# Kernel tuning notes

Measured on AMD Instinct MI355X. Metric: run time of the kernel, lower is better.

Reference implementation:

```python
import jax, jax.numpy as jnp
import numpy as np

P, M, N, H, B, E, K = 50, 512, 1024, 256, 8, 400, 5
ALPHA_MAX, TAU_MAX, RHO_MAX, ETA_MAX = 0.01, 1.0, 1.0, 1.0
LEAK = 0.01  # F.leaky_relu default slope


def _lrelu(x):
    return jnp.where(x >= 0, x, LEAK * x)


def _layernorm(x, g, b, eps=1e-5):
    mu = jnp.mean(x, axis=-1, keepdims=True)
    var = jnp.mean((x - mu) ** 2, axis=-1, keepdims=True)
    return (x - mu) * jax.lax.rsqrt(var + eps) * g + b


def setup_inputs() -> dict:
    ks = iter(jax.random.split(jax.random.key(0), 16))

    def w(fin, fout):
        return jax.random.normal(next(ks), (fin, fout), jnp.float32) * np.float32(np.sqrt(2.0 / (fin + fout)))

    H4 = 4 * H
    inp = {
        'A': jax.random.normal(next(ks), (1, P, M, N), jnp.float32) * 0.05,
        'b': jax.random.normal(next(ks), (B, P, M, 1), jnp.float32),
        'W1': w(2 * N, H), 'b1': jnp.zeros(H), 'bn1_s': jnp.ones(H), 'bn1_t': jnp.zeros(H),
        'W2': w(H, 2 * H), 'b2': jnp.zeros(2 * H), 'bn2_s': jnp.ones(2 * H), 'bn2_t': jnp.zeros(2 * H),
        'W3': w(2 * H, H4), 'b3': jnp.zeros(H4), 'bn3_s': jnp.ones(H4), 'bn3_t': jnp.zeros(H4),
        'W4': w(H4, H4), 'b4': jnp.zeros(H4), 'bn4_s': jnp.ones(H4), 'bn4_t': jnp.zeros(H4),
        'W5': w(H4, H4), 'b5': jnp.zeros(H4), 'bn5_s': jnp.ones(H4), 'bn5_t': jnp.zeros(H4),
        'ln_g': jnp.ones(H4), 'ln_b': jnp.zeros(H4),
        'Wd1': w(P * H4, H4), 'bd1': jnp.zeros(H4), 'lnd1_g': jnp.ones(H4), 'lnd1_b': jnp.zeros(H4),
        'Wd2': w(H4, 2 * H), 'bd2': jnp.zeros(2 * H), 'lnd2_g': jnp.ones(2 * H), 'lnd2_b': jnp.zeros(2 * H),
        'Wd3': w(2 * H, H), 'bd3': jnp.zeros(H), 'lnd3_g': jnp.ones(H), 'lnd3_b': jnp.zeros(H),
        'Wfc': w(H, 4) * 0.1, 'bfc': jnp.zeros(4),
        'edge_index': jax.random.randint(next(ks), (2, E), 0, P),
    }
    return inp


def reference(A, b, W1, b1, bn1_s, bn1_t, W2, b2, bn2_s, bn2_t, W3, b3, bn3_s, bn3_t,
              W4, b4, bn4_s, bn4_t, W5, b5, bn5_s, bn5_t, ln_g, ln_b,
              Wd1, bd1, lnd1_g, lnd1_b, Wd2, bd2, lnd2_g, lnd2_b, Wd3, bd3, lnd3_g, lnd3_b,
              Wfc, bfc, edge_index):
    A0 = A[0]                                             # [P,M,N]
    AtA = jnp.einsum('pmi,pmj->pij', A0, A0)              # [P,N,N]  (compute_Atx(A))
    Atb = jnp.einsum('pmn,bpm->bpn', A0, b[..., 0])[..., None]  # [B,P,N,1]

    src, dst = edge_index[0], edge_index[1]
    ones_e = jnp.ones((E,), A.dtype)
    # sum_neighbors: out-degree of each node p, shape broadcastable to [B,P,1,1]
    sum_nb = jax.ops.segment_sum(ones_e, src, num_segments=P)[None, :, None, None]

    # GCNConv normalization with self loops: norm_ij = deg_i^-1/2 * deg_j^-1/2
    sl = jnp.arange(P)
    src_a = jnp.concatenate([src, sl])
    dst_a = jnp.concatenate([dst, sl])
    deg = jax.ops.segment_sum(jnp.ones((E + P,), A.dtype), dst_a, num_segments=P)
    dinv = jax.lax.rsqrt(deg)
    coef = (dinv[src_a] * dinv[dst_a])[:, None]           # [E+P,1]

    convs = [(W1, b1, bn1_s, bn1_t), (W2, b2, bn2_s, bn2_t), (W3, b3, bn3_s, bn3_t),
             (W4, b4, bn4_s, bn4_t), (W5, b5, bn5_s, bn5_t)]

    def gconv(x, W, bias):                                # x: [P,Cin]
        xw = x @ W
        return jax.ops.segment_sum(xw[src_a] * coef, dst_a, num_segments=P) + bias

    def encode_one(feat):                                 # feat: [P,2N]
        x = feat
        for (W, bias, s, t) in convs:
            # leaky_relu -> BatchNorm1d (eval: affine scale/shift) -> dropout (eval: id)
            x = _lrelu(gconv(x, W, bias)) * s + t
        return _layernorm(x, ln_g, ln_b).reshape(-1)      # [P*4H]

    enc = jax.vmap(encode_one)

    y = jnp.zeros((B, P, N, 1), A.dtype)
    U = jnp.zeros_like(y)
    delta = jnp.zeros_like(y)
    Ys = []
    for k in range(K):
        AtAy = jnp.einsum('pij,bpj->bpi', AtA, y[..., 0])[..., None]  # [B,P,N,1]
        feat = jnp.concatenate([AtAy, Atb], axis=2)[..., 0]           # [B,P,2N]
        code = enc(feat)                                              # [B,P*4H]
        h = _lrelu(_layernorm(code @ Wd1 + bd1, lnd1_g, lnd1_b))
        h = _lrelu(_layernorm(h @ Wd2 + bd2, lnd2_g, lnd2_b))
        h = _lrelu(_layernorm(h @ Wd3 + bd3, lnd3_g, lnd3_b))
        hyp = jnp.clip(jax.nn.sigmoid(h @ Wfc + bfc), 1e-4, 0.99).reshape(B, 4, 1, 1, 1)
        alpha = hyp[:, 0] * ALPHA_MAX
        tau = hyp[:, 1] * TAU_MAX
        rho = hyp[:, 2] * RHO_MAX
        eta = hyp[:, 3] * ETA_MAX
        g = AtAy - Atb + jnp.sign(y) * tau + U * sum_nb + delta * rho
        mg = max(30.0, 100.0 - k)
        g = jnp.clip(g, -mg, mg)
        mv = max(10.0, 200.0 - k * 3)
        y = jnp.clip(y - alpha * g, -mv, mv)
        # compute_delta: for each directed edge (s,d): delta[s]+= (y_s-y_d); delta[d]-= (y_s-y_d)
        diff = y[:, src] - y[:, dst]                                  # [B,E,N,1]
        delta = jnp.zeros_like(y).at[:, src].add(diff).at[:, dst].add(-diff)
        U = jnp.clip(U + delta * eta, -mv, mv)
        Ys.append(y)
    return jnp.stack(Ys)                                              # [K,B,P,N,1]
```

## Files before the change

### kernel.cpp

```cpp
#include <hip/hip_runtime.h>

#define PP 50
#define MM 512
#define NN 1024

constexpr size_t F_ATB   = 0;
constexpr size_t F_ATAY  = F_ATB   + 409600;
constexpr size_t F_Y     = F_ATAY  + 409600;
constexpr size_t F_U     = F_Y     + 409600;
constexpr size_t F_DELTA = F_U     + 409600;
constexpr size_t F_BT    = F_DELTA + 409600;
constexpr size_t F_AYT   = F_BT    + 204800;
constexpr size_t F_ZA    = F_AYT   + 204800;
constexpr size_t F_ZB    = F_ZA    + 458752;
constexpr size_t F_X0    = F_ZB    + 458752;
constexpr size_t F_X1    = F_X0    + 409600;
constexpr size_t F_CODET = F_X1    + 409600;
constexpr size_t F_PART  = F_CODET + 409600;
constexpr size_t F_DPART2= F_PART  + 3670016;
constexpr size_t F_H1    = F_DPART2+ 32768;
constexpr size_t F_H2    = F_H1    + 8192;
constexpr size_t F_H3    = F_H2    + 4096;
constexpr size_t F_HYP   = F_H3    + 2048;
constexpr size_t F_GCCO  = F_HYP   + 64;
constexpr size_t F_SUMNB = F_GCCO  + 512;
constexpr size_t F_W1B   = F_SUMNB + 64;
constexpr size_t F_END   = F_W1B   + 102400;

__device__ __forceinline__ float lrelu(float v) { return v >= 0.f ? v : 0.01f * v; }

__device__ __forceinline__ void bred2(float& s1, float& s2, float* sm) {
  #pragma unroll
  for (int off = 32; off > 0; off >>= 1) {
    s1 += __shfl_down(s1, off);
    s2 += __shfl_down(s2, off);
  }
  int w = threadIdx.x >> 6, l = threadIdx.x & 63;
  if (l == 0) { sm[w] = s1; sm[4 + w] = s2; }
  __syncthreads();
  s1 = sm[0] + sm[1] + sm[2] + sm[3];
  s2 = sm[4] + sm[5] + sm[6] + sm[7];
}

__global__ __launch_bounds__(512) void ksetup(const int* __restrict__ ei, float* sumnb,
                                              float* gccoef, int* gcoff, int* gcsrc,
                                              int* nbroff, int* nbridx) {
  __shared__ int cin[PP];
  __shared__ int cou[PP];
  __shared__ float sdinv[PP];
  __shared__ int goff[PP + 1], noff[PP + 1];
  int t = threadIdx.x;
  const int* src = ei;
  const int* dst = ei + 400;
  if (t < PP) { cin[t] = 0; cou[t] = 0; }
  __syncthreads();
  if (t < 400) {
    atomicAdd(&cou[src[t]], 1);
    atomicAdd(&cin[dst[t]], 1);
  }
  __syncthreads();
  if (t < PP) {
    sdinv[t] = rsqrtf((float)(cin[t] + 1));
    sumnb[t] = (float)cou[t];
  }
  __syncthreads();
  if (t == 0) {
    goff[0] = 0; noff[0] = 0;
    for (int p = 0; p < PP; ++p) {
      goff[p + 1] = goff[p] + cin[p] + 1;
      noff[p + 1] = noff[p] + cin[p] + cou[p];
    }
  }
  __syncthreads();
  if (t <= PP) { gcoff[t] = goff[t]; nbroff[t] = noff[t]; }
  if (t < 400) {
    int d = dst[t], s = src[t];
    int slot = 0;
    for (int e = 0; e < t; ++e) slot += (dst[e] == d) ? 1 : 0;
    int pos = goff[d] + slot;
    gcsrc[pos] = s;
    gccoef[pos] = sdinv[s] * sdinv[d];
  }
  if (t < PP) {
    int pos = goff[t] + cin[t];
    gcsrc[pos] = t;
    gccoef[pos] = sdinv[t] * sdinv[t];
  }
  if (t < 400) {
    int s = src[t], d = dst[t];
    int so = 0, si = 0;
    for (int e = 0; e < t; ++e) {
      so += (src[e] == s) ? 1 : 0;
      si += (dst[e] == d) ? 1 : 0;
    }
    nbridx[noff[s] + so] = d;
    nbridx[noff[d] + cou[d] + si] = s;
  }
}

__global__ __launch_bounds__(256) void kbt(const float* __restrict__ b, float* __restrict__ bt) {
  int i = blockIdx.x * 256 + threadIdx.x;
  int bb = i / (PP * MM);
  int r = i - bb * (PP * MM);
  bt[r * 8 + bb] = b[i];
}

__global__ __launch_bounds__(256) void katz(const float* __restrict__ A, const float* __restrict__ q,
                                            float* __restrict__ outv) {
  __shared__ float red[4][64][8];
  int nb = blockIdx.x, p = blockIdx.y, t = threadIdx.x;
  int ln = t & 63, mg = t >> 6;
  int n = nb * 64 + ln;
  float acc[8] = {0, 0, 0, 0, 0, 0, 0, 0};
  const float* ap = A + ((size_t)p * MM + mg * 128) * NN + n;
  const float* qp = q + ((size_t)p * MM + mg * 128) * 8;
  for (int m0 = 0; m0 < 128; m0 += 8) {
    float av[8];
    #pragma unroll
    for (int u = 0; u < 8; ++u) av[u] = ap[(size_t)(m0 + u) * NN];
    #pragma unroll
    for (int u = 0; u < 8; ++u) {
      #pragma unroll
      for (int bb = 0; bb < 8; ++bb) acc[bb] += av[u] * qp[(m0 + u) * 8 + bb];
    }
  }
  #pragma unroll
  for (int bb = 0; bb < 8; ++bb) red[mg][ln][bb] = acc[bb];
  __syncthreads();
  if (mg == 0) {
    #pragma unroll
    for (int bb = 0; bb < 8; ++bb) {
      float v = red[0][ln][bb] + red[1][ln][bb] + red[2][ln][bb] + red[3][ln][bb];
      outv[((size_t)bb * PP + p) * NN + n] = v;
    }
  }
}

__global__ __launch_bounds__(256) void kay(const float* __restrict__ A, const float* __restrict__ y,
                                           float* __restrict__ ayt) {
  __shared__ __align__(16) float sy[8][NN];
  int p = blockIdx.x, mb = blockIdx.y, t = threadIdx.x;
  #pragma unroll
  for (int bb = 0; bb < 8; ++bb)
    for (int n = t; n < NN; n += 256) sy[bb][n] = y[(bb * PP + p) * NN + n];
  __syncthreads();
  int w = t >> 6, l = t & 63;
  int mbase = mb * 64 + w * 16;
  for (int i = 0; i < 8; ++i) {
    int m0 = mbase + 2 * i, m1 = m0 + 1;
    float acc0[8] = {0, 0, 0, 0, 0, 0, 0, 0};
    float acc1[8] = {0, 0, 0, 0, 0, 0, 0, 0};
    const float* a0p = A + ((size_t)p * MM + m0) * NN;
    const float* a1p = a0p + NN;
    #pragma unroll
    for (int jj = 0; jj < 4; ++jj) {
      int n0 = 4 * l + 256 * jj;
      float4 a0 = *(const float4*)(a0p + n0);
      float4 a1 = *(const float4*)(a1p + n0);
      #pragma unroll
      for (int bb = 0; bb < 8; ++bb) {
        float4 yv = *(const float4*)&sy[bb][n0];
        acc0[bb] += a0.x * yv.x + a0.y * yv.y + a0.z * yv.z + a0.w * yv.w;
        acc1[bb] += a1.x * yv.x + a1.y * yv.y + a1.z * yv.z + a1.w * yv.w;
      }
    }
    #pragma unroll
    for (int off = 32; off > 0; off >>= 1) {
      #pragma unroll
      for (int bb = 0; bb < 8; ++bb) {
        acc0[bb] += __shfl_down(acc0[bb], off);
        acc1[bb] += __shfl_down(acc1[bb], off);
      }
    }
    if (l == 0) {
      #pragma unroll
      for (int bb = 0; bb < 8; ++bb) {
        ayt[((size_t)p * MM + m0) * 8 + bb] = acc0[bb];
        ayt[((size_t)p * MM + m1) * 8 + bb] = acc1[bb];
      }
    }
  }
}

__global__ __launch_bounds__(256) void kgatherX(const float* __restrict__ x, float* __restrict__ z,
                                                int Cin, const int* __restrict__ gcoff,
                                                const int* __restrict__ gcsrc,
                                                const float* __restrict__ gccoef) {
  int r = blockIdx.x, cc = blockIdx.y, t = threadIdx.x;
  int c = cc * 256 + t;
  size_t zi = (size_t)r * Cin + c;
  if (r >= 400) { z[zi] = 0.f; return; }
  int b = r / 50, p = r - b * 50;
  float acc = 0.f;
  int o0 = gcoff[p], o1 = gcoff[p + 1];
  for (int idx = o0; idx < o1; ++idx)
    acc += gccoef[idx] * x[((size_t)b * 50 + gcsrc[idx]) * Cin + c];
  z[zi] = acc;
}

__global__ __launch_bounds__(256) void kgemm(const float* __restrict__ X, const float* __restrict__ W,
                                             float* __restrict__ part, int K, int C, int krange) {
  int cb = blockIdx.x, rb = blockIdx.y, s = blockIdx.z;
  int t = threadIdx.x;
  __shared__ __align__(16) float As[16][64];
  __shared__ __align__(16) float Bs[16][68];
  int rbase = rb * 64, cbase = cb * 64;
  int k0 = s * krange, kend = k0 + krange;
  float acc[4][4] = {};
  int tx = t & 15, ty = t >> 4;
  int lrow = t >> 2, lk = (t & 3) * 4;
  int brow = t >> 4, bc = (t & 15) * 4;
  for (int k = k0; k < kend; k += 16) {
    float4 av = *(const float4*)(X + (size_t)(rbase + lrow) * K + k + lk);
    As[lk + 0][lrow] = av.x;
    As[lk + 1][lrow] = av.y;
    As[lk + 2][lrow] = av.z;
    As[lk + 3][lrow] = av.w;
    *(float4*)&Bs[brow][bc] = *(const float4*)(W + (size_t)(k + brow) * C + cbase + bc);
    __syncthreads();
    #pragma unroll
    for (int kk = 0; kk < 16; ++kk) {
      float4 a = *(const float4*)&As[kk][ty * 4];
      float4 b = *(const float4*)&Bs[kk][tx * 4];
      float aa[4] = {a.x, a.y, a.z, a.w};
      float bb[4] = {b.x, b.y, b.z, b.w};
      #pragma unroll
      for (int i = 0; i < 4; ++i)
        #pragma unroll
        for (int j = 0; j < 4; ++j) acc[i][j] += aa[i] * bb[j];
    }
    __syncthreads();
  }
  #pragma unroll
  for (int i = 0; i < 4; ++i) {
    int r = rbase + ty * 4 + i;
    *(float4*)&part[((size_t)s * 448 + r) * C + cbase + tx * 4] =
        make_float4(acc[i][0], acc[i][1], acc[i][2], acc[i][3]);
  }
}

__global__ __launch_bounds__(256) void kgemmC(const float* __restrict__ XA, const float* __restrict__ XB,
                                              const float* __restrict__ W, float* __restrict__ part,
                                              int C, int krange, int koff) {
  int cb = blockIdx.x, rb = blockIdx.y, s = blockIdx.z;
  int t = threadIdx.x;
  __shared__ __align__(16) float As[16][64];
  __shared__ __align__(16) float Bs[16][68];
  int rbase = rb * 64, cbase = cb * 64;
  int k0 = koff + s * krange, kend = k0 + krange;
  float acc[4][4] = {};
  int tx = t & 15, ty = t >> 4;
  int lrow = t >> 2, lk = (t & 3) * 4;
  int brow = t >> 4, bc = (t & 15) * 4;
  for (int k = k0; k < kend; k += 16) {
    int r = rbase + lrow;
    const float* xp = (k < 1024) ? (XA + (size_t)r * 1024 + k)
                                 : (XB + (size_t)r * 1024 + (k - 1024));
    float4 av = *(const float4*)(xp + lk);
    As[lk + 0][lrow] = av.x;
    As[lk + 1][lrow] = av.y;
    As[lk + 2][lrow] = av.z;
    As[lk + 3][lrow] = av.w;
    *(float4*)&Bs[brow][bc] = *(const float4*)(W + (size_t)(k + brow) * C + cbase + bc);
    __syncthreads();
    #pragma unroll
    for (int kk = 0; kk < 16; ++kk) {
      float4 a = *(const float4*)&As[kk][ty * 4];
      float4 b = *(const float4*)&Bs[kk][tx * 4];
      float aa[4] = {a.x, a.y, a.z, a.w};
      float bb[4] = {b.x, b.y, b.z, b.w};
      #pragma unroll
      for (int i = 0; i < 4; ++i)
        #pragma unroll
        for (int j = 0; j < 4; ++j) acc[i][j] += aa[i] * bb[j];
    }
    __syncthreads();
  }
  #pragma unroll
  for (int i = 0; i < 4; ++i) {
    int r = rbase + ty * 4 + i;
    *(float4*)&part[((size_t)s * 448 + r) * C + cbase + tx * 4] =
        make_float4(acc[i][0], acc[i][1], acc[i][2], acc[i][3]);
  }
}

__global__ __launch_bounds__(256) void kredBase(const float* __restrict__ part,
                                                float* __restrict__ w1b) {
  int r = blockIdx.x, t = threadIdx.x;
  float acc = 0.f;
  #pragma unroll
  for (int s = 0; s < 8; ++s) acc += part[((size_t)s * 448 + r) * 256 + t];
  w1b[(size_t)r * 256 + t] = acc;
}

template <int NCH, bool LASTLN>
__global__ __launch_bounds__(256) void kredE(const float* __restrict__ part, int S,
                                             const float* __restrict__ bias,
                                             const float* __restrict__ bns,
                                             const float* __restrict__ bnt,
                                             float* __restrict__ xout,
                                             const float* __restrict__ lng,
                                             const float* __restrict__ lnb,
                                             float* __restrict__ codet,
                                             const float* __restrict__ base) {
  __shared__ float smr[8];
  constexpr int C = NCH * 256;
  int r = blockIdx.x, t = threadIdx.x;
  float vals[NCH];
  #pragma unroll
  for (int ch = 0; ch < NCH; ++ch) {
    int c = ch * 256 + t;
    float acc = base ? base[(size_t)r * C + c] : 0.f;
    const float* pp = part + (size_t)r * C + c;
    #pragma unroll 4
    for (int s = 0; s < S; ++s) acc += pp[(size_t)s * 448 * C];
    float v = lrelu(acc + bias[c]);
    vals[ch] = v * bns[c] + bnt[c];
  }
  if (!LASTLN) {
    #pragma unroll
    for (int ch = 0; ch < NCH; ++ch)
      xout[(size_t)r * C + ch * 256 + t] = vals[ch];
  } else {
    float s1 = 0.f, s2 = 0.f;
    #pragma unroll
    for (int ch = 0; ch < NCH; ++ch) { s1 += vals[ch]; s2 += vals[ch] * vals[ch]; }
    bred2(s1, s2, smr);
    float mu = s1 / (float)C;
    float var = s2 / (float)C - mu * mu;
    float rs = rsqrtf(var + 1e-5f);
    int b = r / 50, p = r - b * 50;
    #pragma unroll
    for (int ch = 0; ch < NCH; ++ch) {
      int c = ch * 256 + t;
      codet[((size_t)p * C + c) * 8 + b] = (vals[ch] - mu) * rs * lng[c] + lnb[c];
    }
  }
}

__global__ __launch_bounds__(256) void kwd1(const float* __restrict__ W,
                                            const float* __restrict__ in_t,
                                            float* __restrict__ dpart) {
  int t = threadIdx.x, s = blockIdx.x;
  int k0 = s * 200;
  float4 acc[8];
  #pragma unroll
  for (int b = 0; b < 8; ++b) acc[b] = make_float4(0.f, 0.f, 0.f, 0.f);
  const float* wp = W + (size_t)k0 * 1024 + 4 * t;
  const float* qp = in_t + (size_t)k0 * 8;
  for (int k = 0; k < 200; k += 4) {
    float4 wv[4], qa[4], qb[4];
    #pragma unroll
    for (int u = 0; u < 4; ++u) {
      wv[u] = *(const float4*)(wp + (size_t)(k + u) * 1024);
      qa[u] = *(const float4*)(qp + (k + u) * 8);
      qb[u] = *(const float4*)(qp + (k + u) * 8 + 4);
    }
    #pragma unroll
    for (int u = 0; u < 4; ++u) {
      float qs[8] = {qa[u].x, qa[u].y, qa[u].z, qa[u].w, qb[u].x, qb[u].y, qb[u].z, qb[u].w};
      #pragma unroll
      for (int b = 0; b < 8; ++b) {
        acc[b].x += wv[u].x * qs[b];
        acc[b].y += wv[u].y * qs[b];
        acc[b].z += wv[u].z * qs[b];
        acc[b].w += wv[u].w * qs[b];
      }
    }
  }
  #pragma unroll
  for (int b = 0; b < 8; ++b)
    *(float4*)&dpart[(size_t)(s * 8 + b) * 1024 + 4 * t] = acc[b];
}

__global__ __launch_bounds__(256) void kredA(const float* __restrict__ dpart,
                                             float* __restrict__ dpart2) {
  int cb = blockIdx.x, sg = blockIdx.y, b = blockIdx.z, t = threadIdx.x;
  int c = cb * 256 + t;
  float acc = 0.f;
  const float* pp = dpart + ((size_t)(sg * 64) * 8 + b) * 1024 + c;
  #pragma unroll 8
  for (int i = 0; i < 64; ++i) acc += pp[(size_t)i * 8 * 1024];
  dpart2[((size_t)sg * 8 + b) * 1024 + c] = acc;
}

__global__ __launch_bounds__(128) void kwdS(const float* __restrict__ W,
                                            const float* __restrict__ in_t,
                                            float* __restrict__ part, int C, int krange) {
  int t = threadIdx.x, s = blockIdx.x;
  int k0 = s * krange;
  float4 acc[8];
  #pragma unroll
  for (int b = 0; b < 8; ++b) acc[b] = make_float4(0.f, 0.f, 0.f, 0.f);
  const float* wp = W + (size_t)k0 * C + 4 * t;
  const float* qp = in_t + (size_t)k0 * 8;
  for (int k = 0; k < krange; ++k) {
    float4 wv = *(const float4*)(wp + (size_t)k * C);
    float4 qa = *(const float4*)(qp + k * 8);
    float4 qb = *(const float4*)(qp + k * 8 + 4);
    float qs[8] = {qa.x, qa.y, qa.z, qa.w, qb.x, qb.y, qb.z, qb.w};
    #pragma unroll
    for (int b = 0; b < 8; ++b) {
      acc[b].x += wv.x * qs[b];
      acc[b].y += wv.y * qs[b];
      acc[b].z += wv.z * qs[b];
      acc[b].w += wv.w * qs[b];
    }
  }
  #pragma unroll
  for (int b = 0; b < 8; ++b)
    *(float4*)&part[(size_t)(s * 8 + b) * C + 4 * t] = acc[b];
}

__global__ __launch_bounds__(1024) void kred(const float* __restrict__ part, int S, int C,
                                             const float* __restrict__ bias,
                                             const float* __restrict__ g,
                                             const float* __restrict__ be,
                                             float* __restrict__ out_t) {
  __shared__ float sm[32];
  int b = blockIdx.x, t = threadIdx.x;
  float v = bias[t];
  const float* pp = part + (size_t)b * C + t;
  #pragma unroll 4
  for (int s = 0; s < S; ++s) v += pp[(size_t)s * 8 * C];
  float s1 = v, s2 = v * v;
  #pragma unroll
  for (int off = 32; off > 0; off >>= 1) {
    s1 += __shfl_down(s1, off);
    s2 += __shfl_down(s2, off);
  }
  int w = t >> 6, l = t & 63;
  int nw = blockDim.x >> 6;
  if (l == 0) { sm[w] = s1; sm[16 + w] = s2; }
  __syncthreads();
  s1 = 0.f; s2 = 0.f;
  for (int i = 0; i < nw; ++i) { s1 += sm[i]; s2 += sm[16 + i]; }
  float inv = 1.f / (float)C;
  float mu = s1 * inv;
  float var = s2 * inv - mu * mu;
  float rs = rsqrtf(var + 1e-5f);
  float o = lrelu((v - mu) * rs * g[t] + be[t]);
  out_t[t * 8 + b] = o;
}

__global__ __launch_bounds__(256) void kwfc(const float* __restrict__ Wfc, const float* __restrict__ bfc,
                                            const float* __restrict__ h3t, float* __restrict__ hyp) {
  __shared__ float sd[32][257];
  int t = threadIdx.x;
  float4 w = *(const float4*)(Wfc + t * 4);
  #pragma unroll
  for (int bb = 0; bb < 8; ++bb) {
    float x = h3t[t * 8 + bb];
    sd[bb * 4 + 0][t] = x * w.x;
    sd[bb * 4 + 1][t] = x * w.y;
    sd[bb * 4 + 2][t] = x * w.z;
    sd[bb * 4 + 3][t] = x * w.w;
  }
  __syncthreads();
  if (t < 32) {
    float s = 0.f;
    for (int i = 0; i < 256; ++i) s += sd[t][i];
    s += bfc[t & 3];
    float sig = 1.f / (1.f + expf(-s));
    sig = fminf(fmaxf(sig, 1e-4f), 0.99f);
    hyp[t] = sig;
  }
}

__global__ __launch_bounds__(256) void kyupd(const float* __restrict__ atay, const float* __restrict__ atb,
                                             float* y, const float* __restrict__ U,
                                             const float* __restrict__ delta,
                                             const float* __restrict__ hyp,
                                             const float* __restrict__ sumnb, float* __restrict__ outp,
                                             float mg, float mv, int first) {
  int i = blockIdx.x * 256 + threadIdx.x;
  int bb = i / (PP * NN);
  int rem = i - bb * (PP * NN);
  int p = rem >> 10;
  float alpha = hyp[bb * 4 + 0] * 0.01f;
  float g, yv;
  if (first) {
    yv = 0.f;
    g = -atb[i];
  } else {
    float tau = hyp[bb * 4 + 1];
    float rho = hyp[bb * 4 + 2];
    yv = y[i];
    float sg = (yv > 0.f) ? 1.f : ((yv < 0.f) ? -1.f : 0.f);
    g = atay[i] - atb[i] + sg * tau + U[i] * sumnb[p] + delta[i] * rho;
  }
  g = fminf(fmaxf(g, -mg), mg);
  float yn = yv - alpha * g;
  yn = fminf(fmaxf(yn, -mv), mv);
  y[i] = yn;
  outp[i] = yn;
}

__global__ __launch_bounds__(256) void kdeltaU(const float* __restrict__ y, float* __restrict__ delta,
                                               float* __restrict__ U, const float* __restrict__ hyp,
                                               const int* __restrict__ nbroff,
                                               const int* __restrict__ nbridx, float mv, int first) {
  int t = threadIdx.x;
  int n = blockIdx.x * 256 + t;
  int p = blockIdx.y;
  int bb = blockIdx.z;
  int o0 = nbroff[p], o1 = nbroff[p + 1];
  int base = bb * (PP * NN) + p * NN;
  float d = (float)(o1 - o0) * y[base + n];
  for (int idx = o0; idx < o1; ++idx) {
    int q = nbridx[idx];
    d -= y[bb * (PP * NN) + q * NN + n];
  }
  delta[base + n] = d;
  float eta = hyp[bb * 4 + 3];
  float u0 = first ? 0.f : U[base + n];
  float u = u0 + d * eta;
  U[base + n] = fminf(fmaxf(u, -mv), mv);
}

extern "C" void kernel_launch(void* const* d_in, const int* in_sizes, int n_in,
                              void* d_out, int out_size, void* d_ws, size_t ws_size,
                              hipStream_t stream) {
  const float* A    = (const float*)d_in[0];
  const float* bvec = (const float*)d_in[1];
  const float* W1 = (const float*)d_in[2];
  const float* b1 = (const float*)d_in[3];
  const float* bn1s = (const float*)d_in[4];
  const float* bn1t = (const float*)d_in[5];
  const float* W2 = (const float*)d_in[6];
  const float* b2 = (const float*)d_in[7];
  const float* bn2s = (const float*)d_in[8];
  const float* bn2t = (const float*)d_in[9];
  const float* W3 = (const float*)d_in[10];
  const float* b3 = (const float*)d_in[11];
  const float* bn3s = (const float*)d_in[12];
  const float* bn3t = (const float*)d_in[13];
  const float* W4 = (const float*)d_in[14];
  const float* b4 = (const float*)d_in[15];
  const float* bn4s = (const float*)d_in[16];
  const float* bn4t = (const float*)d_in[17];
  const float* W5 = (const float*)d_in[18];
  const float* b5 = (const float*)d_in[19];
  const float* bn5s = (const float*)d_in[20];
  const float* bn5t = (const float*)d_in[21];
  const float* lng = (const float*)d_in[22];
  const float* lnb = (const float*)d_in[23];
  const float* Wd1 = (const float*)d_in[24];
  const float* bd1 = (const float*)d_in[25];
  const float* lnd1g = (const float*)d_in[26];
  const float* lnd1b = (const float*)d_in[27];
  const float* Wd2 = (const float*)d_in[28];
  const float* bd2 = (const float*)d_in[29];
  const float* lnd2g = (const float*)d_in[30];
  const float* lnd2b = (const float*)d_in[31];
  const float* Wd3 = (const float*)d_in[32];
  const float* bd3 = (const float*)d_in[33];
  const float* lnd3g = (const float*)d_in[34];
  const float* lnd3b = (const float*)d_in[35];
  const float* Wfc = (const float*)d_in[36];
  const float* bfc = (const float*)d_in[37];
  const int* ei = (const int*)d_in[38];

  float* out = (float*)d_out;
  float* wsf = (float*)d_ws;
  float* atb = wsf + F_ATB;
  float* atay = wsf + F_ATAY;
  float* yb = wsf + F_Y;
  float* Ub = wsf + F_U;
  float* db = wsf + F_DELTA;
  float* bt = wsf + F_BT;
  float* ayt = wsf + F_AYT;
  float* zA = wsf + F_ZA;
  float* zB = wsf + F_ZB;
  float* x0 = wsf + F_X0;
  float* x1 = wsf + F_X1;
  float* codet = wsf + F_CODET;
  float* part = wsf + F_PART;
  float* dpart = part;
  float* dpart2 = wsf + F_DPART2;
  float* h1t = wsf + F_H1;
  float* h2t = wsf + F_H2;
  float* h3t = wsf + F_H3;
  float* hyp = wsf + F_HYP;
  float* gccoef = wsf + F_GCCO;
  float* sumnb = wsf + F_SUMNB;
  float* w1b = wsf + F_W1B;
  int* wsi = (int*)(wsf + F_END);
  int* gcoff = wsi;
  int* gcsrc = wsi + 64;
  int* nbroff = wsi + 576;
  int* nbridx = wsi + 640;

  ksetup<<<1, 512, 0, stream>>>(ei, sumnb, gccoef, gcoff, gcsrc, nbroff, nbridx);
  kbt<<<800, 256, 0, stream>>>(bvec, bt);
  katz<<<dim3(16, 50), 256, 0, stream>>>(A, bt, atb);
  kgatherX<<<dim3(448, 4), 256, 0, stream>>>(atb, zB, 1024, gcoff, gcsrc, gccoef);
  kgemmC<<<dim3(4, 7, 8), 256, 0, stream>>>(zB, zB, W1, part, 256, 128, 1024);
  kredBase<<<400, 256, 0, stream>>>(part, w1b);

  const float mgs[5] = {100.f, 99.f, 98.f, 97.f, 96.f};
  const float mvs[5] = {200.f, 197.f, 194.f, 191.f, 188.f};

  for (int k = 0; k < 5; ++k) {
    if (k > 0) {
      kay<<<dim3(50, 8), 256, 0, stream>>>(A, yb, ayt);
      katz<<<dim3(16, 50), 256, 0, stream>>>(A, ayt, atay);
    }
    if (k == 0) {
      kredE<1, false><<<400, 256, 0, stream>>>(part, 0, b1, bn1s, bn1t, x0,
                                               nullptr, nullptr, nullptr, w1b);
    } else {
      kgatherX<<<dim3(448, 4), 256, 0, stream>>>(atay, zA, 1024, gcoff, gcsrc, gccoef);
      kgemm<<<dim3(4, 7, 8), 256, 0, stream>>>(zA, W1, part, 1024, 256, 128);
      kredE<1, false><<<400, 256, 0, stream>>>(part, 8, b1, bn1s, bn1t, x0,
                                               nullptr, nullptr, nullptr, w1b);
    }
    kgatherX<<<dim3(448, 1), 256, 0, stream>>>(x0, zA, 256, gcoff, gcsrc, gccoef);
    kgemm<<<dim3(8, 7, 8), 256, 0, stream>>>(zA, W2, part, 256, 512, 32);
    kredE<2, false><<<400, 256, 0, stream>>>(part, 8, b2, bn2s, bn2t, x1,
                                             nullptr, nullptr, nullptr, nullptr);
    kgatherX<<<dim3(448, 2), 256, 0, stream>>>(x1, zA, 512, gcoff, gcsrc, gccoef);
    kgemm<<<dim3(16, 7, 8), 256, 0, stream>>>(zA, W3, part, 512, 1024, 64);
    kredE<4, false><<<400, 256, 0, stream>>>(part, 8, b3, bn3s, bn3t, x0,
                                             nullptr, nullptr, nullptr, nullptr);
    kgatherX<<<dim3(448, 4), 256, 0, stream>>>(x0, zA, 1024, gcoff, gcsrc, gccoef);
    kgemm<<<dim3(16, 7, 8), 256, 0, stream>>>(zA, W4, part, 1024, 1024, 128);
    kredE<4, false><<<400, 256, 0, stream>>>(part, 8, b4, bn4s, bn4t, x1,
                                             nullptr, nullptr, nullptr, nullptr);
    kgatherX<<<dim3(448, 4), 256, 0, stream>>>(x1, zA, 1024, gcoff, gcsrc, gccoef);
    kgemm<<<dim3(16, 7, 8), 256, 0, stream>>>(zA, W5, part, 1024, 1024, 128);
    kredE<4, true><<<400, 256, 0, stream>>>(part, 8, b5, bn5s, bn5t, nullptr,
                                            lng, lnb, codet, nullptr);
    kwd1<<<256, 256, 0, stream>>>(Wd1, codet, dpart);
    kredA<<<dim3(4, 4, 8), 256, 0, stream>>>(dpart, dpart2);
    kred<<<8, 1024, 0, stream>>>(dpart2, 4, 1024, bd1, lnd1g, lnd1b, h1t);
    kwdS<<<64, 128, 0, stream>>>(Wd2, h1t, dpart, 512, 16);
    kred<<<8, 512, 0, stream>>>(dpart, 64, 512, bd2, lnd2g, lnd2b, h2t);
    kwdS<<<32, 64, 0, stream>>>(Wd3, h2t, dpart, 256, 16);
    kred<<<8, 256, 0, stream>>>(dpart, 32, 256, bd3, lnd3g, lnd3b, h3t);
    kwfc<<<1, 256, 0, stream>>>(Wfc, bfc, h3t, hyp);
    kyupd<<<1600, 256, 0, stream>>>(atay, atb, yb, Ub, db, hyp, sumnb,
                                    out + (size_t)k * 409600, mgs[k], mvs[k], k == 0);
    kdeltaU<<<dim3(4, 50, 8), 256, 0, stream>>>(yb, db, Ub, hyp, nbroff, nbridx, mvs[k], k == 0);
  }
}
```

Measured before the change: 1.538 ms.

## Fuse A·y and Aᵀ·(Ay) into one kernel reusing A tiles from cache

```diff
diff --git a/kernel.cpp b/kernel.cpp
--- a/kernel.cpp
+++ b/kernel.cpp
@@ -136,50 +136,88 @@
   }
 }
 
-__global__ __launch_bounds__(256) void kay(const float* __restrict__ A, const float* __restrict__ y,
-                                           float* __restrict__ ayt) {
+__global__ __launch_bounds__(256) void katay2(const float* __restrict__ A,
+                                              const float* __restrict__ y,
+                                              float* __restrict__ part) {
   __shared__ __align__(16) float sy[8][NN];
-  int p = blockIdx.x, mb = blockIdx.y, t = threadIdx.x;
-  #pragma unroll
-  for (int bb = 0; bb < 8; ++bb)
-    for (int n = t; n < NN; n += 256) sy[bb][n] = y[(bb * PP + p) * NN + n];
-  __syncthreads();
+  __shared__ float ss[16][8];
+  int mg = blockIdx.x, p = blockIdx.y, t = threadIdx.x;
   int w = t >> 6, l = t & 63;
-  int mbase = mb * 64 + w * 16;
-  for (int i = 0; i < 8; ++i) {
-    int m0 = mbase + 2 * i, m1 = m0 + 1;
-    float acc0[8] = {0, 0, 0, 0, 0, 0, 0, 0};
-    float acc1[8] = {0, 0, 0, 0, 0, 0, 0, 0};
-    const float* a0p = A + ((size_t)p * MM + m0) * NN;
-    const float* a1p = a0p + NN;
-    #pragma unroll
-    for (int jj = 0; jj < 4; ++jj) {
-      int n0 = 4 * l + 256 * jj;
-      float4 a0 = *(const float4*)(a0p + n0);
-      float4 a1 = *(const float4*)(a1p + n0);
+  for (int idx = t; idx < 8 * NN; idx += 256) {
+    int bb = idx >> 10, n = idx & 1023;
+    sy[bb][n] = y[((size_t)bb * PP + p) * NN + n];
+  }
+  int nco = w * 256 + 4 * l;
+  float4 acc[8];
+  #pragma unroll
+  for (int b = 0; b < 8; ++b) acc[b] = make_float4(0.f, 0.f, 0.f, 0.f);
+  const float* Ab = A + ((size_t)p * MM + (size_t)mg * 64) * NN;
+  __syncthreads();
+  for (int ch = 0; ch < 4; ++ch) {
+    int mbase = ch * 16;
+    #pragma unroll
+    for (int i = 0; i < 4; i += 2) {
+      int r0 = w * 4 + i;
+      const float* a0p = Ab + (size_t)(mbase + r0) * NN;
+      const float* a1p = a0p + NN;
+      float acc0[8] = {0, 0, 0, 0, 0, 0, 0, 0};
+      float acc1[8] = {0, 0, 0, 0, 0, 0, 0, 0};
+      #pragma unroll
+      for (int jj = 0; jj < 4; ++jj) {
+        int n0 = 4 * l + 256 * jj;
+        float4 a0 = *(const float4*)(a0p + n0);
+        float4 a1 = *(const float4*)(a1p + n0);
+        #pragma unroll
+        for (int bb = 0; bb < 8; ++bb) {
+          float4 yv = *(const float4*)&sy[bb][n0];
+          acc0[bb] += a0.x * yv.x + a0.y * yv.y + a0.z * yv.z + a0.w * yv.w;
+          acc1[bb] += a1.x * yv.x + a1.y * yv.y + a1.z * yv.z + a1.w * yv.w;
+        }
+      }
+      #pragma unroll
+      for (int off = 32; off > 0; off >>= 1) {
+        #pragma unroll
+        for (int bb = 0; bb < 8; ++bb) {
+          acc0[bb] += __shfl_down(acc0[bb], off);
+          acc1[bb] += __shfl_down(acc1[bb], off);
+        }
+      }
+      if (l == 0) {
+        #pragma unroll
+        for (int bb = 0; bb < 8; ++bb) {
+          ss[r0][bb] = acc0[bb];
+          ss[r0 + 1][bb] = acc1[bb];
+        }
+      }
+    }
+    __syncthreads();
+    #pragma unroll
+    for (int m = 0; m < 16; ++m) {
+      float4 av = *(const float4*)(Ab + (size_t)(mbase + m) * NN + nco);
       #pragma unroll
       for (int bb = 0; bb < 8; ++bb) {
-        float4 yv = *(const float4*)&sy[bb][n0];
-        acc0[bb] += a0.x * yv.x + a0.y * yv.y + a0.z * yv.z + a0.w * yv.w;
-        acc1[bb] += a1.x * yv.x + a1.y * yv.y + a1.z * yv.z + a1.w * yv.w;
+        float s = ss[m][bb];
+        acc[bb].x += s * av.x;
+        acc[bb].y += s * av.y;
+        acc[bb].z += s * av.z;
+        acc[bb].w += s * av.w;
       }
     }
-    #pragma unroll
-    for (int off = 32; off > 0; off >>= 1) {
-      #pragma unroll
-      for (int bb = 0; bb < 8; ++bb) {
-        acc0[bb] += __shfl_down(acc0[bb], off);
-        acc1[bb] += __shfl_down(acc1[bb], off);
-      }
-    }
-    if (l == 0) {
-      #pragma unroll
-      for (int bb = 0; bb < 8; ++bb) {
-        ayt[((size_t)p * MM + m0) * 8 + bb] = acc0[bb];
-        ayt[((size_t)p * MM + m1) * 8 + bb] = acc1[bb];
-      }
-    }
-  }
+    __syncthreads();
+  }
+  size_t base = (size_t)mg * 409600;
+  #pragma unroll
+  for (int bb = 0; bb < 8; ++bb)
+    *(float4*)&part[base + (((size_t)bb * PP + p) << 10) + nco] = acc[bb];
+}
+
+__global__ __launch_bounds__(256) void kredAtay8(const float* __restrict__ part,
+                                                 float* __restrict__ atay) {
+  int i = blockIdx.x * 256 + threadIdx.x;
+  float v = 0.f;
+  #pragma unroll
+  for (int mg = 0; mg < 8; ++mg) v += part[(size_t)mg * 409600 + i];
+  atay[i] = v;
 }
 
 __global__ __launch_bounds__(256) void kgatherX(const float* __restrict__ x, float* __restrict__ z,
@@ -569,7 +607,6 @@
   float* Ub = wsf + F_U;
   float* db = wsf + F_DELTA;
   float* bt = wsf + F_BT;
-  float* ayt = wsf + F_AYT;
   float* zA = wsf + F_ZA;
   float* zB = wsf + F_ZB;
   float* x0 = wsf + F_X0;
@@ -603,8 +640,8 @@
 
   for (int k = 0; k < 5; ++k) {
     if (k > 0) {
-      kay<<<dim3(50, 8), 256, 0, stream>>>(A, yb, ayt);
-      katz<<<dim3(16, 50), 256, 0, stream>>>(A, ayt, atay);
+      katay2<<<dim3(8, 50), 256, 0, stream>>>(A, yb, part);
+      kredAtay8<<<1600, 256, 0, stream>>>(part, atay);
     }
     if (k == 0) {
       kredE<1, false><<<400, 256, 0, stream>>>(part, 0, b1, bn1s, bn1t, x0,
```

Measured after the change: 1.455 ms. -5.4%, faster.
